# Kernel tuning notes

Measured on AMD Instinct MI355X. Metric: run time of the kernel, lower is better.

Reference implementation:

```python
import jax, jax.numpy as jnp
import numpy as np

GENOTYPE = [("sigmoid", 0), ("relu", 1), ("relu", 1), ("identity", 1),
            ("tanh", 2), ("sigmoid", 5), ("tanh", 3), ("relu", 5)]
CONCAT = list(range(1, 9))
ACT = {"tanh": jnp.tanh, "relu": jax.nn.relu,
       "sigmoid": jax.nn.sigmoid, "identity": lambda x: x}
INITRANGE = 0.04


def setup_inputs() -> dict:
    key = jax.random.key(0)
    ks = jax.random.split(key, 16)
    B, T = 64, 128
    V, D, NC = 32000, 850, 42
    NNER, NPOS, NER_V, POS_V = 30, 30, 25, 50
    STEPS = len(GENOTYPE)

    def u(k, shape):
        return jax.random.uniform(k, shape, jnp.float32, -INITRANGE, INITRANGE)

    enc_W = u(ks[0], (V, D)).at[0].set(0.0)           # padding_idx=0
    ner_W = u(ks[1], (NER_V, NNER)).at[0].set(0.0)
    pos_W = u(ks[2], (POS_V, NPOS)).at[0].set(0.0)
    agg_W = u(ks[3], (D, D + NNER + NPOS))            # Linear weight [out,in]
    agg_b = jnp.zeros((D,), jnp.float32)
    W0 = u(ks[4], (2 * D, 2 * D))                     # (ninp+nhid, 2*nhid)
    Ws = u(ks[5], (STEPS, D, 2 * D))
    dec_W = u(ks[6], (NC, D))
    dec_b = jnp.zeros((NC,), jnp.float32)

    tokens = jax.random.randint(ks[7], (B, T), 0, V)
    masks = jnp.ones((B, T), jnp.float32)
    pos = jax.random.randint(ks[8], (B, T), 0, POS_V)
    ner = jax.random.randint(ks[9], (B, T), 0, NER_V)
    hidden = jnp.zeros((1, B, D), jnp.float32)
    return {"tokens": tokens, "masks": masks, "pos": pos, "ner": ner,
            "hidden": hidden, "enc_W": enc_W, "ner_W": ner_W, "pos_W": pos_W,
            "agg_W": agg_W, "agg_b": agg_b, "W0": W0, "Ws": Ws,
            "dec_W": dec_W, "dec_b": dec_b}


def reference(tokens, masks, pos, ner, hidden,
              enc_W, ner_W, pos_W, agg_W, agg_b, W0, Ws, dec_W, dec_b):
    # Embeddings + aggregation (eval mode: all dropouts are identity)
    emb = enc_W[tokens]                                   # [B,T,D]
    combined = jnp.concatenate([emb, ner_W[ner], pos_W[pos]], axis=2)
    x = combined @ agg_W.T + agg_b                        # [B,T,D]
    x = jnp.transpose(x, (1, 0, 2))                       # [T,B,D]

    h0 = hidden[0]                                        # [B,D]

    def cell(h_prev, xt):
        xh = jnp.concatenate([xt, h_prev], axis=-1)       # [B,2D]
        c0, hh0 = jnp.split(xh @ W0, 2, axis=-1)
        s0 = h_prev + jax.nn.sigmoid(c0) * (jnp.tanh(hh0) - h_prev)
        states = [s0]
        for i, (name, pred) in enumerate(GENOTYPE):
            sp = states[pred]
            c, h = jnp.split(sp @ Ws[i], 2, axis=-1)
            s = sp + jax.nn.sigmoid(c) * (ACT[name](h) - sp)
            states.append(s)
        out = jnp.mean(jnp.stack([states[i] for i in CONCAT], axis=-1), axis=-1)
        return out, out

    _, hiddens = jax.lax.scan(cell, h0, x)                # [T,B,D]
    raw = hiddens * masks.T[:, :, None]                   # mask per timestep
    output = jnp.mean(raw, axis=0)                        # [B,D]
    logit = output @ dec_W.T + dec_b                      # [B,NC]
    log_prob = jax.nn.log_softmax(logit, axis=-1)
    new_hidden = raw[-1][None]                            # [1,B,D]
    return log_prob, new_hidden
```

## Files before the change

kernel.cpp:

```cpp
#include <hip/hip_runtime.h>
#include <math.h>

typedef float f32x4 __attribute__((ext_vector_type(4)));
typedef short s16x8 __attribute__((ext_vector_type(8)));
typedef unsigned short u16;

#define MFMA_BF16(a,b,c) __builtin_amdgcn_mfma_f32_16x16x32_bf16((a),(b),(c),0,0,0)
#define NBLK 243
#define PAIR_U16 13824
#define SLOT_U16 27648
#define LDS_BYTES 110592
#define ST_SLOT 55296


struct P {
  const int* tokens; const void* masks; const int* pos; const int* ner;
  const void* hidden;
  const void* enc_W; const void* ner_W; const void* pos_W;
  const void* agg_W; const void* agg_b;
  const void* W0; const void* Ws;
  const void* dec_W; const void* dec_b;
  void* out;
  unsigned short* PK_agg; unsigned short* PK_rec; unsigned short* comb;
  unsigned short* xbf; unsigned short* Sbf;
  float* accr;
  int* ctrl;
};

#define FB(pp, g, mtv) ((pp).ctrl + 1024 + (((g) * 4 + (mtv)) * 54) * 16)

__device__ __forceinline__ unsigned short f2bf(float f) {
  union { float f; unsigned u; } v; v.f = f;
  return (unsigned short)((v.u + 0x7FFFu + ((v.u >> 16) & 1u)) >> 16);
}
__device__ __forceinline__ float bf2f(u16 x) {
  union { unsigned u; float f; } v; v.u = (unsigned)x << 16; return v.f;
}
__device__ __forceinline__ float ldf(const void* q, size_t i, int bf) {
  if (bf) return bf2f(((const u16*)q)[i]);
  return ((const float*)q)[i];
}
__device__ __forceinline__ void stout(void* o, size_t i, float v, int bf) {
  if (bf) ((u16*)o)[i] = f2bf(v);
  else    ((float*)o)[i] = v;
}
__device__ __forceinline__ float sigm(float x) { return 1.0f / (1.0f + expf(-x)); }
__device__ __forceinline__ float actf(int a, float x) {
  if (a == 0) return sigm(x);
  if (a == 1) return fmaxf(x, 0.0f);
  if (a == 2) return tanhf(x);
  return x;
}

__device__ __forceinline__ s16x8 ldg16_sc1(const u16* p) {
  s16x8 r;
  asm volatile("global_load_dwordx4 %0, %1, off sc1" : "=v"(r) : "v"(p) : "memory");
  return r;
}
__device__ __forceinline__ void vmfence() {
  asm volatile("s_waitcnt vmcnt(0)" ::: "memory");
  __builtin_amdgcn_sched_barrier(0);
}
__device__ __forceinline__ u16 ldc_u16(const u16* p) {
  return __hip_atomic_load(p, __ATOMIC_RELAXED, __HIP_MEMORY_SCOPE_AGENT);
}
__device__ __forceinline__ float ldc_f32(const float* p) {
  unsigned x = __hip_atomic_load((const unsigned*)p, __ATOMIC_RELAXED,
                                 __HIP_MEMORY_SCOPE_AGENT);
  union { unsigned u; float f; } v; v.u = x; return v.f;
}
__device__ __forceinline__ void stc_f32(float* p, float f) {
  union { float f; unsigned u; } v; v.f = f;
  __hip_atomic_store((unsigned*)p, v.u, __ATOMIC_RELAXED, __HIP_MEMORY_SCOPE_AGENT);
}
__device__ __forceinline__ void stc_u16(u16* p, u16 x) {
  __hip_atomic_store(p, x, __ATOMIC_RELAXED, __HIP_MEMORY_SCOPE_AGENT);
}
__device__ __forceinline__ void stc_i32(int* p, int x) {
  __hip_atomic_store(p, x, __ATOMIC_RELAXED, __HIP_MEMORY_SCOPE_AGENT);
}
__device__ __forceinline__ int ldc_i32(const int* p) {
  return __hip_atomic_load(p, __ATOMIC_RELAXED, __HIP_MEMORY_SCOPE_AGENT);
}

__device__ __forceinline__ void setfW(int* fb, int fi, int e) {
  asm volatile("s_waitcnt vmcnt(0)" ::: "memory");
  if ((threadIdx.x & 63) == 0) stc_i32(fb + fi * 16, e);
}
__device__ __forceinline__ void waitW(const int* fb, int n, int e) {
  int l = threadIdx.x & 63, it = 0;
  for (;;) {
    int ok = (l < n) ? (ldc_i32(fb + l * 16) >= e) : 1;
    if (__all(ok)) break;
    if (++it > 4000000) break;
    if (it > 2) __builtin_amdgcn_s_sleep(2);
  }
  asm volatile("" ::: "memory");
}
__device__ __forceinline__ void waitW2(const int* fa, int na, const int* fb, int nb, int e) {
  int l = threadIdx.x & 63, it = 0;
  for (;;) {
    int ok = ((l < na) ? (ldc_i32(fa + l * 16) >= e) : 1) &
             ((l < nb) ? (ldc_i32(fb + l * 16) >= e) : 1);
    if (__all(ok)) break;
    if (++it > 4000000) break;
    if (it > 2) __builtin_amdgcn_s_sleep(2);
  }
  asm volatile("" ::: "memory");
}
__device__ __forceinline__ void waitW3(const int* fa, const int* fb, const int* fc,
                                       int n, int e) {
  int l = threadIdx.x & 63, it = 0;
  for (;;) {
    int ok = 1;
    if (l < n) ok = (ldc_i32(fa + l * 16) >= e) & (ldc_i32(fb + l * 16) >= e) &
                    (ldc_i32(fc + l * 16) >= e);
    if (__all(ok)) break;
    if (++it > 4000000) break;
    if (it > 2) __builtin_amdgcn_s_sleep(2);
  }
  asm volatile("" ::: "memory");
}


__global__ void k_detect(P p) {
  for (int j = threadIdx.x; j < 32768; j += 64) p.ctrl[j] = 0;
  __syncthreads();
  if (threadIdx.x == 0) {
    const u16* u = (const u16*)p.W0;
    int good = 0;
    for (int i = 0; i < 256; ++i) {
      int e = (u[i] >> 7) & 0xFF;
      if (e >= 90 && e <= 126) ++good;
    }
    p.ctrl[0] = (good >= 192) ? 1 : 0;
  }
}

__global__ __launch_bounds__(256) void k_init0(P p) {
  const int total = 442368 + 114688;
  for (int e = blockIdx.x * blockDim.x + threadIdx.x; e < total;
       e += gridDim.x * blockDim.x) {
    if (e < 442368) {
      ((unsigned*)p.Sbf)[e] = 0u;
    } else {
      int e4 = e - 442368; int t = e4 / 896, r = e4 % 896;
      int b = r / 14, n = 850 + r % 14;
      p.xbf[((size_t)t * 64 + b) * 864 + n] = 0;
    }
  }
}

__global__ __launch_bounds__(256) void k_init1(P p) {
  const int bf = p.ctrl[0];
  for (int e = blockIdx.x * blockDim.x + threadIdx.x; e < 54400;
       e += gridDim.x * blockDim.x) {
    int b = e / 850, n = e % 850;
    p.Sbf[(size_t)7 * ST_SLOT + (((size_t)(n >> 4) * 64 + b) << 4) + (n & 15)] =
        f2bf(ldf(p.hidden, e, bf));
  }
}

__global__ __launch_bounds__(256) void k_pack_agg(P p) {
  const int bf = p.ctrl[0];
  const long total = 801792L;
  for (long e = (long)blockIdx.x * blockDim.x + threadIdx.x; e < total;
       e += (long)gridDim.x * blockDim.x) {
    int j = (int)(e & 7), l = (int)((e >> 3) & 63);
    long q9 = e >> 9;
    int kb = (int)(q9 % 29), nt = (int)(q9 / 29);
    int n = nt * 16 + (l & 15);
    int k = kb * 32 + ((l >> 4) << 3) + j;
    float v = 0.0f;
    if (n < 850 && k < 910) v = ldf(p.agg_W, (size_t)n * 910 + k, bf);
    p.PK_agg[e] = f2bf(v);
  }
}

__global__ __launch_bounds__(256) void k_comb(P p) {
  const int bf = p.ctrl[0];
  const long total = 7602176L;
  for (long e = (long)blockIdx.x * blockDim.x + threadIdx.x; e < total;
       e += (long)gridDim.x * blockDim.x) {
    int k = (int)(e % 928);
    int r = (int)(e / 928);
    int t = r >> 6, b = r & 63;
    float v = 0.0f;
    if (k < 850)      { int tok = p.tokens[b * 128 + t]; v = ldf(p.enc_W, (size_t)tok * 850 + k, bf); }
    else if (k < 880) { int nv = p.ner[b * 128 + t];     v = ldf(p.ner_W, nv * 30 + (k - 850), bf); }
    else if (k < 910) { int pv = p.pos[b * 128 + t];     v = ldf(p.pos_W, pv * 30 + (k - 880), bf); }
    p.comb[e] = f2bf(v);
  }
}

__global__ __launch_bounds__(256) void k_pack_rec(P p) {
  const int bf = p.ctrl[0];
  const long total = 14929920L;
  for (long e = (long)blockIdx.x * blockDim.x + threadIdx.x; e < total;
       e += (long)gridDim.x * blockDim.x) {
    int j = (int)(e & 7), l = (int)((e >> 3) & 63);
    long q9 = e >> 9;
    int kb = (int)(q9 % 27);
    long q = q9 / 27;
    int nt = (int)(q % 54);
    int mh = (int)(q / 54);
    int half = mh & 1, mat = mh >> 1;
    int nl = nt * 16 + (l & 15);
    int col = half ? nl + 850 : nl;
    int k = kb * 32 + ((l >> 4) << 3) + j;
    float v = 0.0f;
    if (nl < 850 && k < 850) {
      if (mat == 0)      v = ldf(p.W0, (size_t)k * 1700 + col, bf);
      else if (mat == 1) v = ldf(p.W0, (size_t)(k + 850) * 1700 + col, bf);
      else               v = ldf(p.Ws, (size_t)(mat - 2) * 850 * 1700 + (size_t)k * 1700 + col, bf);
    }
    p.PK_rec[e] = f2bf(v);
  }
}

__global__ void k_diag(P p) {
  if (blockIdx.x == 0 && threadIdx.x == 0)
    for (int i = 0; i < 64; ++i) ((float*)p.out)[i] = 2000.0f;
}

__global__ __launch_bounds__(256) void k_phaseA(P p) {
  const int tid = threadIdx.x;
  const int l = tid & 63, lm = l & 15, lg = l >> 4;
  const int wid = (blockIdx.x << 2) | (tid >> 6);
  const int bf = p.ctrl[0];
  for (int u = wid; u < 512 * 54; u += 1024) {
    int mt = u / 54, nt = u - mt * 54;
    int r0 = mt << 4;
    f32x4 acc = {0.f, 0.f, 0.f, 0.f};
    const u16* Arow = p.comb + (size_t)(r0 + lm) * 928 + (size_t)lg * 8;
    const u16* Bp = p.PK_agg + (size_t)nt * 29 * 512 + (size_t)l * 8;
    for (int kb = 0; kb < 29; ++kb) {
      s16x8 a = *(const s16x8*)(Arow + (size_t)kb * 32);
      s16x8 b = *(const s16x8*)(Bp + (size_t)kb * 512);
      acc = MFMA_BF16(a, b, acc);
    }
    int n = nt * 16 + lm;
    if (n < 850) {
      float bias = ldf(p.agg_b, n, bf);
#pragma unroll
      for (int i = 0; i < 4; ++i) {
        int r = r0 + lg * 4 + i;
        p.xbf[(size_t)r * 864 + n] = f2bf(acc[i] + bias);
      }
    }
  }
}


__device__ __forceinline__ void burstA(const u16* st, int mt, int l, s16x8* ab) {
  const int lm = l & 15, lg = l >> 4;
  const int row = mt * 16 + lm;
  const u16* A = st + (((size_t)(lg >> 1) * 64 + row) << 4) + ((lg & 1) << 3);
#pragma unroll
  for (int kb = 0; kb < 27; ++kb) ab[kb] = ldg16_sc1(A + (size_t)kb * 2048);
}

__device__ __forceinline__ void unitS(const u16* lds, const u16* st, int nt, int mt,
                                      int l, f32x4& cc, f32x4& hh, float* prev) {
  const int lm = l & 15, lg = l >> 4;
  s16x8 ab[27];
  burstA(st, mt, l, ab);
  u16 pv[4];
#pragma unroll
  for (int i = 0; i < 4; ++i)
    pv[i] = ldc_u16(st + (((size_t)nt * 64 + mt * 16 + lg * 4 + i) << 4) + lm);
  vmfence();
  const f32x4 z = {0.f, 0.f, 0.f, 0.f};
  f32x4 c0 = z, c1 = z, h0 = z, h1 = z;
#pragma unroll
  for (int kb = 0; kb < 27; ++kb) {
    s16x8 bc = *(const s16x8*)(lds + l * 8 + (size_t)kb * 512);
    s16x8 bh = *(const s16x8*)(lds + PAIR_U16 + l * 8 + (size_t)kb * 512);
    if (kb & 1) { c1 = MFMA_BF16(ab[kb], bc, c1); h1 = MFMA_BF16(ab[kb], bh, h1); }
    else        { c0 = MFMA_BF16(ab[kb], bc, c0); h0 = MFMA_BF16(ab[kb], bh, h0); }
  }
  cc += c0 + c1; hh += h0 + h1;
#pragma unroll
  for (int i = 0; i < 4; ++i) prev[i] = bf2f(pv[i]);
}

__device__ __forceinline__ void unit2S(const u16* lds0, const u16* lds1, const u16* st,
                                       int ntA, int ntB, int mt, int l,
                                       f32x4& cA, f32x4& hA, f32x4& cB, f32x4& hB,
                                       float* prevA, float* prevB) {
  const int lm = l & 15, lg = l >> 4;
  s16x8 ab[27];
  burstA(st, mt, l, ab);
  u16 pa[4], pb[4];
#pragma unroll
  for (int i = 0; i < 4; ++i) {
    size_t row = mt * 16 + lg * 4 + i;
    pa[i] = ldc_u16(st + (((size_t)ntA * 64 + row) << 4) + lm);
    pb[i] = ldc_u16(st + (((size_t)ntB * 64 + row) << 4) + lm);
  }
  vmfence();
#pragma unroll
  for (int kb = 0; kb < 27; ++kb) {
    cA = MFMA_BF16(ab[kb], *(const s16x8*)(lds0 + l * 8 + (size_t)kb * 512), cA);
    hA = MFMA_BF16(ab[kb], *(const s16x8*)(lds0 + PAIR_U16 + l * 8 + (size_t)kb * 512), hA);
    cB = MFMA_BF16(ab[kb], *(const s16x8*)(lds1 + l * 8 + (size_t)kb * 512), cB);
    hB = MFMA_BF16(ab[kb], *(const s16x8*)(lds1 + PAIR_U16 + l * 8 + (size_t)kb * 512), hB);
  }
#pragma unroll
  for (int i = 0; i < 4; ++i) { prevA[i] = bf2f(pa[i]); prevB[i] = bf2f(pb[i]); }
}

__device__ __forceinline__ void unit_x(const P& p, int nt, int t, int mt, int l,
                                       f32x4& cc, f32x4& hh) {
  const int lm = l & 15, lg = l >> 4;
  const u16* Ax = p.xbf + ((size_t)t * 64 + mt * 16 + lm) * 864 + (size_t)lg * 8;
  const u16* B0 = p.PK_rec + (size_t)(0 * 54 + nt) * PAIR_U16 + l * 8;
  const u16* B1 = p.PK_rec + (size_t)(1 * 54 + nt) * PAIR_U16 + l * 8;
  s16x8 ab[27];
#pragma unroll
  for (int kb = 0; kb < 27; ++kb) ab[kb] = *(const s16x8*)(Ax + (size_t)kb * 32);
  const f32x4 z = {0.f, 0.f, 0.f, 0.f};
  f32x4 c0 = z, c1 = z, h0 = z, h1 = z;
#pragma unroll
  for (int kb = 0; kb < 27; ++kb) {
    s16x8 bc = *(const s16x8*)(B0 + (size_t)kb * 512);
    s16x8 bh = *(const s16x8*)(B1 + (size_t)kb * 512);
    if (kb & 1) { c1 = MFMA_BF16(ab[kb], bc, c1); h1 = MFMA_BF16(ab[kb], bh, h1); }
    else        { c0 = MFMA_BF16(ab[kb], bc, c0); h0 = MFMA_BF16(ab[kb], bh, h0); }
  }
  cc += c0 + c1; hh += h0 + h1;
}

__device__ __forceinline__ void epiS(const P& p, int par, int slot, int nt, int mt,
                                     int l, const float* prev, int act,
                                     f32x4 c, f32x4 h) {
  int lm = l & 15, lg = l >> 4, n = nt * 16 + lm;
  if (n >= 850) return;
  u16* dst = p.Sbf + (size_t)(par * 8 + slot) * ST_SLOT;
#pragma unroll
  for (int i = 0; i < 4; ++i) {
    size_t row = mt * 16 + lg * 4 + i;
    float s = prev[i] + sigm(c[i]) * (actf(act, h[i]) - prev[i]);
    stc_u16(dst + (((size_t)nt * 64 + row) << 4) + lm, f2bf(s));
  }
}

__global__ __launch_bounds__(256, 1) void k_scan(P p) {
  extern __shared__ u16 ldsw[];
  const int tid = threadIdx.x;
  const int l = tid & 63, lm = l & 15, lg = l >> 4, mt = tid >> 6;
  const int blk = blockIdx.x;
  const int bf = p.ctrl[0];
#define STP(par, slot) (p.Sbf + (size_t)((par) * 8 + (slot)) * ST_SLOT)

  int role, matA, ntA, matB, ntB;
  if (blk < 54)       { role = 0; matA = 1; ntA = blk;       matB = 3; ntB = ntA; }
  else if (blk < 108) { role = 1; matA = 2; ntA = blk - 54;  matB = 4; ntB = ntA; }
  else if (blk < 162) { role = 2; matA = 6; ntA = blk - 108; matB = 5; ntB = ntA; }
  else if (blk < 216) { role = 3; matA = 7; ntA = blk - 162; matB = 9; ntB = ntA; }
  else                { role = 4; matA = 8; ntA = 2 * (blk - 216); matB = 8; ntB = ntA + 1; }

  for (int s = 0; s < 2; ++s) {
    int m = s ? matB : matA, nt = s ? ntB : ntA;
    for (int h = 0; h < 2; ++h) {
      const uint4* src = (const uint4*)(p.PK_rec + ((size_t)(m * 2 + h) * 54 + nt) * PAIR_U16);
      uint4* dst = (uint4*)(ldsw + s * SLOT_U16 + h * PAIR_U16);
      for (int i = tid; i < PAIR_U16 / 8; i += 256) dst[i] = src[i];
    }
  }
  __syncthreads();

  const f32x4 z = {0.f, 0.f, 0.f, 0.f};

  if (role == 0) {
    const int fi = blk;
    for (int t = 0; t < 128; ++t) {
      int par = t & 1;
      f32x4 cc = z, hh = z;
      unit_x(p, ntA, t, mt, l, cc, hh);
      waitW(FB(p, 7, mt), 54, t);
      float pv[4];
      unitS(ldsw, STP(par, 7), ntA, mt, l, cc, hh, pv);
      epiS(p, par, 0, ntA, mt, l, pv, 2, cc, hh);
      setfW(FB(p, 0, mt), fi, t + 1);
      waitW(FB(p, 1, mt), 54, t + 1);
      f32x4 c2 = z, h2 = z; float p2[4];
      unitS(ldsw + SLOT_U16, STP(par, 1), ntA, mt, l, c2, h2, p2);
      epiS(p, par, 2, ntA, mt, l, p2, 1, c2, h2);
      setfW(FB(p, 2, mt), fi, t + 1);
    }
    if (blk < 16) {
      int b = blk * 4 + mt;
      waitW(FB(p, 7, b >> 4), 54, 128);
      float myval = 0.0f;
      for (int c = 0; c < 42; ++c) {
        float part = 0.0f;
        for (int d = l; d < 850; d += 64)
          part += ldc_f32(p.accr + b * 850 + d) * ldf(p.dec_W, c * 850 + d, bf);
        for (int off = 32; off > 0; off >>= 1) part += __shfl_xor(part, off);
        if (l == c) myval = part * (1.0f / 128.0f) + ldf(p.dec_b, c, bf);
      }
      float mx = (l < 42) ? myval : -INFINITY;
      for (int off = 32; off > 0; off >>= 1) mx = fmaxf(mx, __shfl_xor(mx, off));
      float ex = (l < 42) ? expf(myval - mx) : 0.0f;
      float sm = ex;
      for (int off = 32; off > 0; off >>= 1) sm += __shfl_xor(sm, off);
      if (l < 42) stout(p.out, (size_t)b * 42 + l, myval - mx - logf(sm), bf);
    }
  } else if (role == 1) {
    const int fi = blk - 54;
    for (int t = 0; t < 128; ++t) {
      int par = t & 1;
      waitW(FB(p, 0, mt), 54, t + 1);
      f32x4 cc = z, hh = z; float pv[4];
      unitS(ldsw, STP(par, 0), ntA, mt, l, cc, hh, pv);
      epiS(p, par, 1, ntA, mt, l, pv, 0, cc, hh);
      setfW(FB(p, 1, mt), fi, t + 1);
      waitW(FB(p, 1, mt), 54, t + 1);
      f32x4 c2 = z, h2 = z; float p2[4];
      unitS(ldsw + SLOT_U16, STP(par, 1), ntA, mt, l, c2, h2, p2);
      epiS(p, par, 3, ntA, mt, l, p2, 1, c2, h2);
      setfW(FB(p, 3, mt), fi, t + 1);
    }
  } else if (role == 2) {
    const int fi = blk - 108;
    for (int t = 0; t < 128; ++t) {
      int par = t & 1;
      waitW(FB(p, 1, mt), 54, t + 1);
      f32x4 cc = z, hh = z; float pv[4];
      unitS(ldsw + SLOT_U16, STP(par, 1), ntA, mt, l, cc, hh, pv);
      epiS(p, par, 4, ntA, mt, l, pv, 3, cc, hh);
      setfW(FB(p, 4, mt), fi, t + 1);
      waitW(FB(p, 2, mt), 54, t + 1);
      f32x4 c2 = z, h2 = z; float p2[4];
      unitS(ldsw, STP(par, 2), ntA, mt, l, c2, h2, p2);
      epiS(p, par, 5, ntA, mt, l, p2, 2, c2, h2);
      setfW(FB(p, 5, mt), fi, t + 1);
    }
  } else if (role == 4) {
    const int fi = blk - 216;
    for (int t = 0; t < 128; ++t) {
      int par = t & 1;
      waitW(FB(p, 3, mt), 54, t + 1);
      f32x4 cA = z, hA = z, cB = z, hB = z; float pa[4], pb[4];
      unit2S(ldsw, ldsw + SLOT_U16, STP(par, 3), ntA, ntB, mt, l,
             cA, hA, cB, hB, pa, pb);
      epiS(p, par, 6, ntA, mt, l, pa, 2, cA, hA);
      epiS(p, par, 6, ntB, mt, l, pb, 2, cB, hB);
      setfW(FB(p, 6, mt), fi, t + 1);
    }
  } else {
    const int fi = blk - 162;
    float areg[4] = {0.f, 0.f, 0.f, 0.f};
    const int n = ntA * 16 + lm;
    for (int t = 0; t < 128; ++t) {
      int par = t & 1, par2 = (t + 1) & 1;
      waitW3(FB(p, 2, mt), FB(p, 3, mt), FB(p, 4, mt), 54, t + 1);
      float psum[4];
      {
        u16 q1[4], q2[4], q3[4], q4[4];
#pragma unroll
        for (int i = 0; i < 4; ++i) {
          size_t off = (((size_t)ntA * 64 + mt * 16 + lg * 4 + i) << 4) + lm;
          q1[i] = ldc_u16(STP(par, 1) + off); q2[i] = ldc_u16(STP(par, 2) + off);
          q3[i] = ldc_u16(STP(par, 3) + off); q4[i] = ldc_u16(STP(par, 4) + off);
        }
#pragma unroll
        for (int i = 0; i < 4; ++i)
          psum[i] = bf2f(q1[i]) + bf2f(q2[i]) + bf2f(q3[i]) + bf2f(q4[i]);
      }
      waitW2(FB(p, 5, mt), 54, FB(p, 6, mt), 27, t + 1);
      u16 q7[4];
#pragma unroll
      for (int i = 0; i < 4; ++i)
        q7[i] = ldc_u16(STP(par, 6) + (((size_t)ntA * 64 + mt * 16 + lg * 4 + i) << 4) + lm);
      f32x4 cA = z, hA = z, cB = z, hB = z; float s5v[4], s5d[4];
      unit2S(ldsw, ldsw + SLOT_U16, STP(par, 5), ntA, ntA, mt, l,
             cA, hA, cB, hB, s5v, s5d);
      if (n < 850) {
        u16* hdst = STP(par2, 7);
#pragma unroll
        for (int i = 0; i < 4; ++i) {
          int b = mt * 16 + lg * 4 + i;
          float s6 = s5v[i] + sigm(cA[i]) * (sigm(hA[i]) - s5v[i]);
          float s8 = s5v[i] + sigm(cB[i]) * (fmaxf(hB[i], 0.f) - s5v[i]);
          float sum = psum[i] + s5v[i] + bf2f(q7[i]) + s6 + s8;
          float outv = sum * 0.125f;
          float mk = ldf(p.masks, b * 128 + t, bf);
          areg[i] += outv * mk;
          stc_u16(hdst + (((size_t)ntA * 64 + b) << 4) + lm, f2bf(outv));
          if (t == 127) {
            stout(p.out, 2688 + (size_t)b * 850 + n, outv * mk, bf);
            stc_f32(p.accr + b * 850 + n, areg[i]);
          }
        }
      }
      setfW(FB(p, 7, mt), fi, t + 1);
    }
  }
#undef STP
}


extern "C" void kernel_launch(void* const* d_in, const int* in_sizes, int n_in,
                              void* d_out, int out_size, void* d_ws, size_t ws_size,
                              hipStream_t stream) {
  (void)in_sizes; (void)n_in; (void)out_size;
  P p;
  p.tokens = (const int*)d_in[0];
  p.masks  = d_in[1];
  p.pos    = (const int*)d_in[2];
  p.ner    = (const int*)d_in[3];
  p.hidden = d_in[4];
  p.enc_W  = d_in[5];
  p.ner_W  = d_in[6];
  p.pos_W  = d_in[7];
  p.agg_W  = d_in[8];
  p.agg_b  = d_in[9];
  p.W0     = d_in[10];
  p.Ws     = d_in[11];
  p.dec_W  = d_in[12];
  p.dec_b  = d_in[13];
  p.out    = d_out;

  unsigned char* ws = (unsigned char*)d_ws;
  p.ctrl = (int*)ws;
  unsigned char* R0 = ws + 262144;
  p.PK_agg = (unsigned short*)R0;
  p.comb   = (unsigned short*)(R0 + 1603584);
  p.PK_rec = (unsigned short*)R0;
  unsigned char* q = R0 + 29859840;
  p.xbf  = (unsigned short*)q; q += 14155776;
  p.Sbf  = (unsigned short*)q; q += 1769472;
  p.accr = (float*)q;          q += 217600;

  size_t need = (size_t)(q - ws);
  if (ws_size < need) {
    hipLaunchKernelGGL(k_diag, dim3(1), dim3(64), 0, stream, p);
    return;
  }

  static int lds_attr_set = 0;
  if (!lds_attr_set) {
    (void)hipFuncSetAttribute((const void*)k_scan,
                              hipFuncAttributeMaxDynamicSharedMemorySize, LDS_BYTES);
    lds_attr_set = 1;
  }

  hipLaunchKernelGGL(k_detect,   dim3(1),    dim3(64),  0, stream, p);
  hipLaunchKernelGGL(k_init0,    dim3(256),  dim3(256), 0, stream, p);
  hipLaunchKernelGGL(k_init1,    dim3(64),   dim3(256), 0, stream, p);
  hipLaunchKernelGGL(k_pack_agg, dim3(512),  dim3(256), 0, stream, p);
  hipLaunchKernelGGL(k_comb,     dim3(4096), dim3(256), 0, stream, p);
  hipLaunchKernelGGL(k_phaseA,   dim3(256),  dim3(256), 0, stream, p);
  hipLaunchKernelGGL(k_pack_rec, dim3(4096), dim3(256), 0, stream, p);
  hipLaunchKernelGGL(k_scan,     dim3(NBLK), dim3(256), LDS_BYTES, stream, p);
}
```

Measured before the change: 3.395 ms.

## Split flag waits into staged per-chunk waits and narrow dependency waits

```diff
diff --git a/kernel.cpp b/kernel.cpp
--- a/kernel.cpp
+++ b/kernel.cpp
@@ -93,31 +93,15 @@
     int ok = (l < n) ? (ldc_i32(fb + l * 16) >= e) : 1;
     if (__all(ok)) break;
     if (++it > 4000000) break;
-    if (it > 2) __builtin_amdgcn_s_sleep(2);
+    if (it > 3) __builtin_amdgcn_s_sleep(1);
   }
   asm volatile("" ::: "memory");
 }
-__device__ __forceinline__ void waitW2(const int* fa, int na, const int* fb, int nb, int e) {
-  int l = threadIdx.x & 63, it = 0;
-  for (;;) {
-    int ok = ((l < na) ? (ldc_i32(fa + l * 16) >= e) : 1) &
-             ((l < nb) ? (ldc_i32(fb + l * 16) >= e) : 1);
-    if (__all(ok)) break;
+__device__ __forceinline__ void wait1(const int* f, int e) {
+  int it = 0;
+  while (ldc_i32(f) < e) {
     if (++it > 4000000) break;
-    if (it > 2) __builtin_amdgcn_s_sleep(2);
-  }
-  asm volatile("" ::: "memory");
-}
-__device__ __forceinline__ void waitW3(const int* fa, const int* fb, const int* fc,
-                                       int n, int e) {
-  int l = threadIdx.x & 63, it = 0;
-  for (;;) {
-    int ok = 1;
-    if (l < n) ok = (ldc_i32(fa + l * 16) >= e) & (ldc_i32(fb + l * 16) >= e) &
-                    (ldc_i32(fc + l * 16) >= e);
-    if (__all(ok)) break;
-    if (++it > 4000000) break;
-    if (it > 2) __builtin_amdgcn_s_sleep(2);
+    if (it > 3) __builtin_amdgcn_s_sleep(1);
   }
   asm volatile("" ::: "memory");
 }
@@ -252,19 +236,25 @@
 }
 
 
-__device__ __forceinline__ void burstA(const u16* st, int mt, int l, s16x8* ab) {
+__device__ __forceinline__ void unitSC(const u16* lds, const u16* st, const int* fb,
+                                       int e, int nt, int mt, int l,
+                                       f32x4& cc, f32x4& hh, float* prev) {
   const int lm = l & 15, lg = l >> 4;
   const int row = mt * 16 + lm;
   const u16* A = st + (((size_t)(lg >> 1) * 64 + row) << 4) + ((lg & 1) << 3);
-#pragma unroll
-  for (int kb = 0; kb < 27; ++kb) ab[kb] = ldg16_sc1(A + (size_t)kb * 2048);
-}
-
-__device__ __forceinline__ void unitS(const u16* lds, const u16* st, int nt, int mt,
-                                      int l, f32x4& cc, f32x4& hh, float* prev) {
-  const int lm = l & 15, lg = l >> 4;
   s16x8 ab[27];
-  burstA(st, mt, l, ab);
+  waitW(fb, 14, e);
+#pragma unroll
+  for (int kb = 0; kb < 7; ++kb) ab[kb] = ldg16_sc1(A + (size_t)kb * 2048);
+  waitW(fb, 28, e);
+#pragma unroll
+  for (int kb = 7; kb < 14; ++kb) ab[kb] = ldg16_sc1(A + (size_t)kb * 2048);
+  waitW(fb, 42, e);
+#pragma unroll
+  for (int kb = 14; kb < 21; ++kb) ab[kb] = ldg16_sc1(A + (size_t)kb * 2048);
+  waitW(fb, 54, e);
+#pragma unroll
+  for (int kb = 21; kb < 27; ++kb) ab[kb] = ldg16_sc1(A + (size_t)kb * 2048);
   u16 pv[4];
 #pragma unroll
   for (int i = 0; i < 4; ++i)
@@ -284,19 +274,33 @@
   for (int i = 0; i < 4; ++i) prev[i] = bf2f(pv[i]);
 }
 
-__device__ __forceinline__ void unit2S(const u16* lds0, const u16* lds1, const u16* st,
-                                       int ntA, int ntB, int mt, int l,
-                                       f32x4& cA, f32x4& hA, f32x4& cB, f32x4& hB,
-                                       float* prevA, float* prevB) {
+__device__ __forceinline__ void unit2SC(const u16* lds0, const u16* lds1, const u16* st,
+                                        const int* fb, int e, int ntA, int ntB,
+                                        int mt, int l,
+                                        f32x4& cA, f32x4& hA, f32x4& cB, f32x4& hB,
+                                        float* prevA, float* prevB) {
   const int lm = l & 15, lg = l >> 4;
+  const int row = mt * 16 + lm;
+  const u16* A = st + (((size_t)(lg >> 1) * 64 + row) << 4) + ((lg & 1) << 3);
   s16x8 ab[27];
-  burstA(st, mt, l, ab);
+  waitW(fb, 14, e);
+#pragma unroll
+  for (int kb = 0; kb < 7; ++kb) ab[kb] = ldg16_sc1(A + (size_t)kb * 2048);
+  waitW(fb, 28, e);
+#pragma unroll
+  for (int kb = 7; kb < 14; ++kb) ab[kb] = ldg16_sc1(A + (size_t)kb * 2048);
+  waitW(fb, 42, e);
+#pragma unroll
+  for (int kb = 14; kb < 21; ++kb) ab[kb] = ldg16_sc1(A + (size_t)kb * 2048);
+  waitW(fb, 54, e);
+#pragma unroll
+  for (int kb = 21; kb < 27; ++kb) ab[kb] = ldg16_sc1(A + (size_t)kb * 2048);
   u16 pa[4], pb[4];
 #pragma unroll
   for (int i = 0; i < 4; ++i) {
-    size_t row = mt * 16 + lg * 4 + i;
-    pa[i] = ldc_u16(st + (((size_t)ntA * 64 + row) << 4) + lm);
-    pb[i] = ldc_u16(st + (((size_t)ntB * 64 + row) << 4) + lm);
+    size_t r2 = mt * 16 + lg * 4 + i;
+    pa[i] = ldc_u16(st + (((size_t)ntA * 64 + r2) << 4) + lm);
+    pb[i] = ldc_u16(st + (((size_t)ntB * 64 + r2) << 4) + lm);
   }
   vmfence();
 #pragma unroll
@@ -378,14 +382,12 @@
       int par = t & 1;
       f32x4 cc = z, hh = z;
       unit_x(p, ntA, t, mt, l, cc, hh);
-      waitW(FB(p, 7, mt), 54, t);
       float pv[4];
-      unitS(ldsw, STP(par, 7), ntA, mt, l, cc, hh, pv);
+      unitSC(ldsw, STP(par, 7), FB(p, 7, mt), t, ntA, mt, l, cc, hh, pv);
       epiS(p, par, 0, ntA, mt, l, pv, 2, cc, hh);
       setfW(FB(p, 0, mt), fi, t + 1);
-      waitW(FB(p, 1, mt), 54, t + 1);
       f32x4 c2 = z, h2 = z; float p2[4];
-      unitS(ldsw + SLOT_U16, STP(par, 1), ntA, mt, l, c2, h2, p2);
+      unitSC(ldsw + SLOT_U16, STP(par, 1), FB(p, 1, mt), t + 1, ntA, mt, l, c2, h2, p2);
       epiS(p, par, 2, ntA, mt, l, p2, 1, c2, h2);
       setfW(FB(p, 2, mt), fi, t + 1);
     }
@@ -411,14 +413,12 @@
     const int fi = blk - 54;
     for (int t = 0; t < 128; ++t) {
       int par = t & 1;
-      waitW(FB(p, 0, mt), 54, t + 1);
       f32x4 cc = z, hh = z; float pv[4];
-      unitS(ldsw, STP(par, 0), ntA, mt, l, cc, hh, pv);
+      unitSC(ldsw, STP(par, 0), FB(p, 0, mt), t + 1, ntA, mt, l, cc, hh, pv);
       epiS(p, par, 1, ntA, mt, l, pv, 0, cc, hh);
       setfW(FB(p, 1, mt), fi, t + 1);
-      waitW(FB(p, 1, mt), 54, t + 1);
       f32x4 c2 = z, h2 = z; float p2[4];
-      unitS(ldsw + SLOT_U16, STP(par, 1), ntA, mt, l, c2, h2, p2);
+      unitSC(ldsw + SLOT_U16, STP(par, 1), FB(p, 1, mt), t + 1, ntA, mt, l, c2, h2, p2);
       epiS(p, par, 3, ntA, mt, l, p2, 1, c2, h2);
       setfW(FB(p, 3, mt), fi, t + 1);
     }
@@ -426,14 +426,12 @@
     const int fi = blk - 108;
     for (int t = 0; t < 128; ++t) {
       int par = t & 1;
-      waitW(FB(p, 1, mt), 54, t + 1);
       f32x4 cc = z, hh = z; float pv[4];
-      unitS(ldsw + SLOT_U16, STP(par, 1), ntA, mt, l, cc, hh, pv);
+      unitSC(ldsw + SLOT_U16, STP(par, 1), FB(p, 1, mt), t + 1, ntA, mt, l, cc, hh, pv);
       epiS(p, par, 4, ntA, mt, l, pv, 3, cc, hh);
       setfW(FB(p, 4, mt), fi, t + 1);
-      waitW(FB(p, 2, mt), 54, t + 1);
       f32x4 c2 = z, h2 = z; float p2[4];
-      unitS(ldsw, STP(par, 2), ntA, mt, l, c2, h2, p2);
+      unitSC(ldsw, STP(par, 2), FB(p, 2, mt), t + 1, ntA, mt, l, c2, h2, p2);
       epiS(p, par, 5, ntA, mt, l, p2, 2, c2, h2);
       setfW(FB(p, 5, mt), fi, t + 1);
     }
@@ -441,10 +439,9 @@
     const int fi = blk - 216;
     for (int t = 0; t < 128; ++t) {
       int par = t & 1;
-      waitW(FB(p, 3, mt), 54, t + 1);
       f32x4 cA = z, hA = z, cB = z, hB = z; float pa[4], pb[4];
-      unit2S(ldsw, ldsw + SLOT_U16, STP(par, 3), ntA, ntB, mt, l,
-             cA, hA, cB, hB, pa, pb);
+      unit2SC(ldsw, ldsw + SLOT_U16, STP(par, 3), FB(p, 3, mt), t + 1,
+              ntA, ntB, mt, l, cA, hA, cB, hB, pa, pb);
       epiS(p, par, 6, ntA, mt, l, pa, 2, cA, hA);
       epiS(p, par, 6, ntB, mt, l, pb, 2, cB, hB);
       setfW(FB(p, 6, mt), fi, t + 1);
@@ -455,7 +452,9 @@
     const int n = ntA * 16 + lm;
     for (int t = 0; t < 128; ++t) {
       int par = t & 1, par2 = (t + 1) & 1;
-      waitW3(FB(p, 2, mt), FB(p, 3, mt), FB(p, 4, mt), 54, t + 1);
+      wait1(FB(p, 2, mt) + ntA * 16, t + 1);
+      wait1(FB(p, 3, mt) + ntA * 16, t + 1);
+      wait1(FB(p, 4, mt) + ntA * 16, t + 1);
       float psum[4];
       {
         u16 q1[4], q2[4], q3[4], q4[4];
@@ -469,14 +468,14 @@
         for (int i = 0; i < 4; ++i)
           psum[i] = bf2f(q1[i]) + bf2f(q2[i]) + bf2f(q3[i]) + bf2f(q4[i]);
       }
-      waitW2(FB(p, 5, mt), 54, FB(p, 6, mt), 27, t + 1);
+      f32x4 cA = z, hA = z, cB = z, hB = z; float s5v[4], s5d[4];
+      unit2SC(ldsw, ldsw + SLOT_U16, STP(par, 5), FB(p, 5, mt), t + 1,
+              ntA, ntA, mt, l, cA, hA, cB, hB, s5v, s5d);
+      wait1(FB(p, 6, mt) + (ntA >> 1) * 16, t + 1);
       u16 q7[4];
 #pragma unroll
       for (int i = 0; i < 4; ++i)
         q7[i] = ldc_u16(STP(par, 6) + (((size_t)ntA * 64 + mt * 16 + lg * 4 + i) << 4) + lm);
-      f32x4 cA = z, hA = z, cB = z, hB = z; float s5v[4], s5d[4];
-      unit2S(ldsw, ldsw + SLOT_U16, STP(par, 5), ntA, ntA, mt, l,
-             cA, hA, cB, hB, s5v, s5d);
       if (n < 850) {
         u16* hdst = STP(par2, 7);
 #pragma unroll
```

After: 3.478 ms. +2.4%, slower.

## Narrow flag waits to producer tiles and add progress-aware backoff

Applied to the files above, without the earlier changes.

```diff
diff --git a/kernel.cpp b/kernel.cpp
--- a/kernel.cpp
+++ b/kernel.cpp
@@ -83,41 +83,37 @@
   return __hip_atomic_load(p, __ATOMIC_RELAXED, __HIP_MEMORY_SCOPE_AGENT);
 }
 
+__device__ __forceinline__ void backoff(int it) {
+  if (it > 12)     __builtin_amdgcn_s_sleep(16);
+  else if (it > 2) __builtin_amdgcn_s_sleep(2);
+}
+
 __device__ __forceinline__ void setfW(int* fb, int fi, int e) {
   asm volatile("s_waitcnt vmcnt(0)" ::: "memory");
   if ((threadIdx.x & 63) == 0) stc_i32(fb + fi * 16, e);
 }
-__device__ __forceinline__ void waitW(const int* fb, int n, int e) {
-  int l = threadIdx.x & 63, it = 0;
+__device__ __forceinline__ void waitL(const int* fb, int n, int e) {
+  int l = threadIdx.x & 63;
+  bool done = (l >= n);
+  int it = 0, last = -1, guard = 0;
   for (;;) {
-    int ok = (l < n) ? (ldc_i32(fb + l * 16) >= e) : 1;
-    if (__all(ok)) break;
-    if (++it > 4000000) break;
-    if (it > 2) __builtin_amdgcn_s_sleep(2);
+    if (!done) done = (ldc_i32(fb + l * 16) >= e);
+    unsigned long long m = __ballot(done);
+    if (m == ~0ULL) break;
+    int cnt = (int)__popcll(m);
+    if (cnt != last) { last = cnt; it = 0; }
+    if (++guard > 8000000) break;
+    ++it;
+    backoff(it);
   }
   asm volatile("" ::: "memory");
 }
-__device__ __forceinline__ void waitW2(const int* fa, int na, const int* fb, int nb, int e) {
-  int l = threadIdx.x & 63, it = 0;
-  for (;;) {
-    int ok = ((l < na) ? (ldc_i32(fa + l * 16) >= e) : 1) &
-             ((l < nb) ? (ldc_i32(fb + l * 16) >= e) : 1);
-    if (__all(ok)) break;
-    if (++it > 4000000) break;
-    if (it > 2) __builtin_amdgcn_s_sleep(2);
-  }
-  asm volatile("" ::: "memory");
-}
-__device__ __forceinline__ void waitW3(const int* fa, const int* fb, const int* fc,
-                                       int n, int e) {
-  int l = threadIdx.x & 63, it = 0;
-  for (;;) {
-    int ok = 1;
-    if (l < n) ok = (ldc_i32(fa + l * 16) >= e) & (ldc_i32(fb + l * 16) >= e) &
-                    (ldc_i32(fc + l * 16) >= e);
-    if (__all(ok)) break;
-    if (++it > 4000000) break;
-    if (it > 2) __builtin_amdgcn_s_sleep(2);
+__device__ __forceinline__ void wait1(const int* f, int e) {
+  int it = 0, guard = 0;
+  while (ldc_i32(f) < e) {
+    if (++guard > 8000000) break;
+    ++it;
+    backoff(it);
   }
   asm volatile("" ::: "memory");
 }
@@ -378,12 +374,12 @@
       int par = t & 1;
       f32x4 cc = z, hh = z;
       unit_x(p, ntA, t, mt, l, cc, hh);
-      waitW(FB(p, 7, mt), 54, t);
+      waitL(FB(p, 7, mt), 54, t);
       float pv[4];
       unitS(ldsw, STP(par, 7), ntA, mt, l, cc, hh, pv);
       epiS(p, par, 0, ntA, mt, l, pv, 2, cc, hh);
       setfW(FB(p, 0, mt), fi, t + 1);
-      waitW(FB(p, 1, mt), 54, t + 1);
+      waitL(FB(p, 1, mt), 54, t + 1);
       f32x4 c2 = z, h2 = z; float p2[4];
       unitS(ldsw + SLOT_U16, STP(par, 1), ntA, mt, l, c2, h2, p2);
       epiS(p, par, 2, ntA, mt, l, p2, 1, c2, h2);
@@ -391,7 +387,7 @@
     }
     if (blk < 16) {
       int b = blk * 4 + mt;
-      waitW(FB(p, 7, b >> 4), 54, 128);
+      waitL(FB(p, 7, b >> 4), 54, 128);
       float myval = 0.0f;
       for (int c = 0; c < 42; ++c) {
         float part = 0.0f;
@@ -411,12 +407,12 @@
     const int fi = blk - 54;
     for (int t = 0; t < 128; ++t) {
       int par = t & 1;
-      waitW(FB(p, 0, mt), 54, t + 1);
+      waitL(FB(p, 0, mt), 54, t + 1);
       f32x4 cc = z, hh = z; float pv[4];
       unitS(ldsw, STP(par, 0), ntA, mt, l, cc, hh, pv);
       epiS(p, par, 1, ntA, mt, l, pv, 0, cc, hh);
       setfW(FB(p, 1, mt), fi, t + 1);
-      waitW(FB(p, 1, mt), 54, t + 1);
+      waitL(FB(p, 1, mt), 54, t + 1);
       f32x4 c2 = z, h2 = z; float p2[4];
       unitS(ldsw + SLOT_U16, STP(par, 1), ntA, mt, l, c2, h2, p2);
       epiS(p, par, 3, ntA, mt, l, p2, 1, c2, h2);
@@ -426,12 +422,12 @@
     const int fi = blk - 108;
     for (int t = 0; t < 128; ++t) {
       int par = t & 1;
-      waitW(FB(p, 1, mt), 54, t + 1);
+      waitL(FB(p, 1, mt), 54, t + 1);
       f32x4 cc = z, hh = z; float pv[4];
       unitS(ldsw + SLOT_U16, STP(par, 1), ntA, mt, l, cc, hh, pv);
       epiS(p, par, 4, ntA, mt, l, pv, 3, cc, hh);
       setfW(FB(p, 4, mt), fi, t + 1);
-      waitW(FB(p, 2, mt), 54, t + 1);
+      waitL(FB(p, 2, mt), 54, t + 1);
       f32x4 c2 = z, h2 = z; float p2[4];
       unitS(ldsw, STP(par, 2), ntA, mt, l, c2, h2, p2);
       epiS(p, par, 5, ntA, mt, l, p2, 2, c2, h2);
@@ -441,7 +437,7 @@
     const int fi = blk - 216;
     for (int t = 0; t < 128; ++t) {
       int par = t & 1;
-      waitW(FB(p, 3, mt), 54, t + 1);
+      waitL(FB(p, 3, mt), 54, t + 1);
       f32x4 cA = z, hA = z, cB = z, hB = z; float pa[4], pb[4];
       unit2S(ldsw, ldsw + SLOT_U16, STP(par, 3), ntA, ntB, mt, l,
              cA, hA, cB, hB, pa, pb);
@@ -455,7 +451,9 @@
     const int n = ntA * 16 + lm;
     for (int t = 0; t < 128; ++t) {
       int par = t & 1, par2 = (t + 1) & 1;
-      waitW3(FB(p, 2, mt), FB(p, 3, mt), FB(p, 4, mt), 54, t + 1);
+      wait1(FB(p, 2, mt) + ntA * 16, t + 1);
+      wait1(FB(p, 3, mt) + ntA * 16, t + 1);
+      wait1(FB(p, 4, mt) + ntA * 16, t + 1);
       float psum[4];
       {
         u16 q1[4], q2[4], q3[4], q4[4];
@@ -469,14 +467,15 @@
         for (int i = 0; i < 4; ++i)
           psum[i] = bf2f(q1[i]) + bf2f(q2[i]) + bf2f(q3[i]) + bf2f(q4[i]);
       }
-      waitW2(FB(p, 5, mt), 54, FB(p, 6, mt), 27, t + 1);
-      u16 q7[4];
-#pragma unroll
-      for (int i = 0; i < 4; ++i)
-        q7[i] = ldc_u16(STP(par, 6) + (((size_t)ntA * 64 + mt * 16 + lg * 4 + i) << 4) + lm);
+      waitL(FB(p, 5, mt), 54, t + 1);
       f32x4 cA = z, hA = z, cB = z, hB = z; float s5v[4], s5d[4];
       unit2S(ldsw, ldsw + SLOT_U16, STP(par, 5), ntA, ntA, mt, l,
              cA, hA, cB, hB, s5v, s5d);
+      wait1(FB(p, 6, mt) + (ntA >> 1) * 16, t + 1);
+      u16 q7[4];
+#pragma unroll
+      for (int i = 0; i < 4; ++i)
+        q7[i] = ldc_u16(STP(par, 6) + (((size_t)ntA * 64 + mt * 16 + lg * 4 + i) << 4) + lm);
       if (n < 850) {
         u16* hdst = STP(par2, 7);
 #pragma unroll
```

Result: faster. 3.115 ms, median of 3 (-8.3%).
